# Performance work log

Measured on AMD Instinct MI355X. Metric: run time of the kernel, lower is better.

Reference implementation:

```python
import jax, jax.numpy as jnp
import numpy as np

NUM_EMBEDDINGS = 1024
EMBEDDING_DIM = 64
BETA = 0.25  # commitment_cost


def setup_inputs() -> dict:
    key = jax.random.key(0)
    k1, k2 = jax.random.split(key)
    z = jax.random.normal(k1, (32, EMBEDDING_DIM, 32, 32), dtype=jnp.float32)
    embedding = jax.random.normal(k2, (NUM_EMBEDDINGS, EMBEDDING_DIM), dtype=jnp.float32)
    return {"z": z, "embedding": embedding}


def reference(z, embedding):
    B, D, H, W = z.shape
    beta = jnp.asarray(BETA, z.dtype)
    # [B, D, H, W] -> [B*H*W, D]
    z_flat = jnp.transpose(z, (0, 2, 3, 1)).reshape(-1, D)
    # squared L2 distances to each code: ||z||^2 - 2 z.e^T + ||e||^2  -> [N, E]
    dist = (
        jnp.sum(z_flat * z_flat, axis=1, keepdims=True)
        - 2.0 * (z_flat @ embedding.T)
        + jnp.sum(embedding * embedding, axis=1)
    )
    encoding_indices = jnp.argmin(dist, axis=1)  # [N]
    # direct gather instead of one-hot matmul (same math)
    quantized = embedding[encoding_indices]  # [N, D]
    quantized = jnp.transpose(quantized.reshape(B, H, W, D), (0, 3, 1, 2))
    commitment_loss = beta * jnp.mean(
        (jax.lax.stop_gradient(z) - quantized) ** 2
    )
    codebook_loss = jnp.mean((z - jax.lax.stop_gradient(quantized)) ** 2)
    loss = commitment_loss + codebook_loss
    # straight-through estimator
    quantized_st = z + jax.lax.stop_gradient(quantized - z)
    return (quantized_st, loss, encoding_indices)
```

## Files before the change

kernel.cpp:

```cpp
#include <hip/hip_runtime.h>

typedef __attribute__((ext_vector_type(8))) short short8;
typedef __attribute__((ext_vector_type(4))) float f32x4;
typedef unsigned int uint32;

#define DMQ 64
#define QOUT 2097152

__device__ __forceinline__ unsigned short f2bf(float f){
  uint32 u = __float_as_uint(f);
  return (unsigned short)((u + 0x7FFFu + ((u >> 16) & 1u)) >> 16);
}
__device__ __forceinline__ float bf2f(unsigned short h){
  return __uint_as_float(((uint32)h) << 16);
}
__device__ __forceinline__ uint32 med3u(uint32 a, uint32 b, uint32 c){
  uint32 d;
  asm("v_med3_u32 %0, %1, %2, %3" : "=v"(d) : "v"(a), "v"(b), "v"(c));
  return d;
}
__device__ __forceinline__ void glds16(const unsigned char* g, unsigned char* l){
  __builtin_amdgcn_global_load_lds(
      (const __attribute__((address_space(1))) unsigned int*)g,
      (__attribute__((address_space(3))) unsigned int*)l, 16, 0, 0);
}

__global__ void vq_prep(const float* __restrict__ emb,
                        unsigned char* __restrict__ ebg,
                        float* __restrict__ nrm64){
  int C = blockIdx.x * 256 + threadIdx.x;
  const float4* e4 = reinterpret_cast<const float4*>(emb + C * DMQ);
  int chunk = C >> 8, cc = C & 255;
  unsigned char* eb = ebg + chunk * 65536;
  int x = (cc & 7) << 1;
  float s = 0.f;
#pragma unroll
  for (int sub = 0; sub < 16; ++sub){
    float4 v = e4[sub];
    s += v.x*v.x + v.y*v.y + v.z*v.z + v.w*v.w;
    ushort4 h, l;
    h.x = f2bf(v.x); l.x = f2bf(v.x - bf2f(h.x));
    h.y = f2bf(v.y); l.y = f2bf(v.y - bf2f(h.y));
    h.z = f2bf(v.z); l.z = f2bf(v.z - bf2f(h.z));
    h.w = f2bf(v.w); l.w = f2bf(v.w - bf2f(h.w));
    int off = cc * 128 + ((sub ^ x) << 3);
    *reinterpret_cast<ushort4*>(eb + off) = h;
    *reinterpret_cast<ushort4*>(eb + 32768 + off) = l;
  }
  nrm64[C] = 0.5f * s + 128.0f;
}

__global__ __launch_bounds__(256, 2) void vq_main(
    const float* __restrict__ z, const float* __restrict__ emb,
    const unsigned char* __restrict__ ebg, const float* __restrict__ nrm64,
    float* __restrict__ out, float* __restrict__ partial)
{
  __shared__ __align__(16) unsigned char LB[65536];
  __shared__ float nrmlds[1024];
  __shared__ uint32 mg[64][2][3];
  __shared__ int kidx[64];
  __shared__ float perr[256];

  const int t = threadIdx.x;
  const int bi = blockIdx.x;
  const int n0 = bi * 64;
  const int b = n0 >> 10;
  const int hw0 = n0 & 1023;
  const int w = t >> 6, lane = t & 63;
  const int wm = w >> 1, wn = w & 1;
  const int l15 = lane & 15, g = lane >> 4;

  for (int i = t; i < 1024; i += 256) nrmlds[i] = nrm64[i];

  float* zf = reinterpret_cast<float*>(LB);
#pragma unroll
  for (int k = 0; k < 16; ++k){
    int li = k * 256 + t;
    int d = li >> 6, j = li & 63;
    zf[j * 68 + d] = z[((b * DMQ + d) << 10) + hw0 + j];
  }
  __syncthreads();

  short8 ah[2][2], al[2][2];
#pragma unroll
  for (int mf = 0; mf < 2; ++mf)
#pragma unroll
    for (int kf = 0; kf < 2; ++kf){
      int row = wm * 32 + mf * 16 + l15;
      int base = row * 68 + kf * 32 + g * 8;
      float4 q0 = *reinterpret_cast<float4*>(&zf[base]);
      float4 q1 = *reinterpret_cast<float4*>(&zf[base + 4]);
      float vv[8] = {q0.x,q0.y,q0.z,q0.w,q1.x,q1.y,q1.z,q1.w};
#pragma unroll
      for (int j = 0; j < 8; ++j){
        float v = -vv[j];
        unsigned short hs = f2bf(v);
        unsigned short ls = f2bf(v - bf2f(hs));
        ah[mf][kf][j] = (short)hs;
        al[mf][kf][j] = (short)ls;
      }
    }
  __syncthreads();

  uint32 u0[8], u1[8], u2[8];
#pragma unroll
  for (int s = 0; s < 8; ++s){ u0[s] = 0xFFFFFFFFu; u1[s] = 0xFFFFFFFFu; u2[s] = 0xFFFFFFFFu; }

  const int cc0 = wn * 128 + l15;
  const int xsw = (l15 & 7) << 1;
  const int v0s = ((g * 2) ^ xsw) << 3;
  const int v1s = ((8 + g * 2) ^ xsw) << 3;

  for (int c = 0; c < 4; ++c){
    const unsigned char* src = ebg + c * 65536;
#pragma unroll
    for (int r = 0; r < 16; ++r){
      int off = (r * 4 + w) * 1024;
      glds16(src + off + lane * 16, LB + off);
    }
    __syncthreads();

#pragma unroll
    for (int nf = 0; nf < 8; ++nf){
      int cc = cc0 + nf * 16;
      const unsigned char* rb = LB + cc * 128;
      short8 bh0 = *reinterpret_cast<const short8*>(rb + v0s);
      short8 bh1 = *reinterpret_cast<const short8*>(rb + v1s);
      short8 bl0 = *reinterpret_cast<const short8*>(rb + 32768 + v0s);
      short8 bl1 = *reinterpret_cast<const short8*>(rb + 32768 + v1s);
      float nv = nrmlds[(c << 8) + cc];
      f32x4 a0 = {nv, nv, nv, nv};
      f32x4 a1 = {nv, nv, nv, nv};
      a0 = __builtin_amdgcn_mfma_f32_16x16x32_bf16(ah[0][0], bh0, a0, 0,0,0);
      a0 = __builtin_amdgcn_mfma_f32_16x16x32_bf16(ah[0][1], bh1, a0, 0,0,0);
      a0 = __builtin_amdgcn_mfma_f32_16x16x32_bf16(al[0][0], bh0, a0, 0,0,0);
      a0 = __builtin_amdgcn_mfma_f32_16x16x32_bf16(al[0][1], bh1, a0, 0,0,0);
      a0 = __builtin_amdgcn_mfma_f32_16x16x32_bf16(ah[0][0], bl0, a0, 0,0,0);
      a0 = __builtin_amdgcn_mfma_f32_16x16x32_bf16(ah[0][1], bl1, a0, 0,0,0);
      a1 = __builtin_amdgcn_mfma_f32_16x16x32_bf16(ah[1][0], bh0, a1, 0,0,0);
      a1 = __builtin_amdgcn_mfma_f32_16x16x32_bf16(ah[1][1], bh1, a1, 0,0,0);
      a1 = __builtin_amdgcn_mfma_f32_16x16x32_bf16(al[1][0], bh0, a1, 0,0,0);
      a1 = __builtin_amdgcn_mfma_f32_16x16x32_bf16(al[1][1], bh1, a1, 0,0,0);
      a1 = __builtin_amdgcn_mfma_f32_16x16x32_bf16(ah[1][0], bl0, a1, 0,0,0);
      a1 = __builtin_amdgcn_mfma_f32_16x16x32_bf16(ah[1][1], bl1, a1, 0,0,0);
      uint32 kb = (uint32)((c << 8) | cc0 | (nf << 4));
#pragma unroll
      for (int r = 0; r < 4; ++r){
        uint32 k0v = (__float_as_uint(a0[r]) & 0xFFFFFC00u) | kb;
        u2[r] = med3u(k0v, u1[r], u2[r]);
        u1[r] = med3u(k0v, u0[r], u1[r]);
        u0[r] = u0[r] < k0v ? u0[r] : k0v;
        uint32 k1v = (__float_as_uint(a1[r]) & 0xFFFFFC00u) | kb;
        u2[4+r] = med3u(k1v, u1[4+r], u2[4+r]);
        u1[4+r] = med3u(k1v, u0[4+r], u1[4+r]);
        u0[4+r] = u0[4+r] < k1v ? u0[4+r] : k1v;
      }
    }
    __syncthreads();
  }

#pragma unroll
  for (int dm = 1; dm < 16; dm <<= 1){
#pragma unroll
    for (int s = 0; s < 8; ++s){
      uint32 x0 = (uint32)__shfl_xor((int)u0[s], dm);
      uint32 x1 = (uint32)__shfl_xor((int)u1[s], dm);
      uint32 x2 = (uint32)__shfl_xor((int)u2[s], dm);
      u2[s] = med3u(x0, u1[s], u2[s]); u1[s] = med3u(x0, u0[s], u1[s]); u0[s] = u0[s] < x0 ? u0[s] : x0;
      u2[s] = med3u(x1, u1[s], u2[s]); u1[s] = med3u(x1, u0[s], u1[s]); u0[s] = u0[s] < x1 ? u0[s] : x1;
      u2[s] = med3u(x2, u1[s], u2[s]); u1[s] = med3u(x2, u0[s], u1[s]); u0[s] = u0[s] < x2 ? u0[s] : x2;
    }
  }
  if (l15 == 0){
#pragma unroll
    for (int mf = 0; mf < 2; ++mf)
#pragma unroll
      for (int r = 0; r < 4; ++r){
        int lr = wm * 32 + mf * 16 + g * 4 + r;
        int s = mf * 4 + r;
        mg[lr][wn][0] = u0[s]; mg[lr][wn][1] = u1[s]; mg[lr][wn][2] = u2[s];
      }
  }
  __syncthreads();

  if (t < 64){
    uint32 a0k = mg[t][0][0], a1k = mg[t][0][1], a2k = mg[t][0][2];
#pragma unroll
    for (int j = 0; j < 3; ++j){
      uint32 x = mg[t][1][j];
      a2k = med3u(x, a1k, a2k); a1k = med3u(x, a0k, a1k); a0k = a0k < x ? a0k : x;
    }
    int k0 = (int)(a0k & 1023u);
    float d0 = __uint_as_float(a0k & 0xFFFFFC00u);
    float d1 = __uint_as_float(a1k & 0xFFFFFC00u);
    if (d1 - d0 < 0.125f){
      int k1 = (int)(a1k & 1023u);
      int k2 = (int)(a2k & 1023u);
      float d2v = __uint_as_float(a2k & 0xFFFFFC00u);
      bool c2 = (d2v - d0 < 0.125f);
      const float* zb = z + (b << 16) + hw0 + t;
      const float* e0 = emb + k0 * DMQ;
      const float* e1 = emb + k1 * DMQ;
      const float* e2 = emb + k2 * DMQ;
      double s0 = 0.0, s1 = 0.0, s2 = 0.0;
      for (int d = 0; d < DMQ; ++d){
        double zd = (double)zb[d << 10];
        double t0 = zd - (double)e0[d]; s0 += t0 * t0;
        double t1 = zd - (double)e1[d]; s1 += t1 * t1;
        double t2 = zd - (double)e2[d]; s2 += t2 * t2;
      }
      int bk = k0; double bs = s0;
      if (s1 < bs || (s1 == bs && k1 < bk)) { bs = s1; bk = k1; }
      if (c2 && (s2 < bs || (s2 == bs && k2 < bk))) { bs = s2; bk = k2; }
      k0 = bk;
    }
    kidx[t] = k0;
    out[QOUT + 1 + n0 + t] = (float)k0;
  }
  __syncthreads();

  {
    int row = t & 63, dp = t >> 6;
    int k = kidx[row];
    const float* e = emb + k * DMQ;
    const float* zb = z + (b << 16) + hw0 + row;
    float* ob = out + (b << 16) + hw0 + row;
    float err = 0.f;
#pragma unroll
    for (int dd = 0; dd < 16; ++dd){
      int d = dp * 16 + dd;
      float zv = zb[d << 10];
      float qv = e[d];
      ob[d << 10] = qv;
      float df = zv - qv;
      err = fmaf(df, df, err);
    }
    perr[t] = err;
  }
  __syncthreads();
  for (int ww = 128; ww > 0; ww >>= 1){
    if (t < ww) perr[t] += perr[t + ww];
    __syncthreads();
  }
  if (t == 0) partial[bi] = perr[0];
}

__global__ void vq_reduce(const float* __restrict__ partial, float* __restrict__ out) {
  __shared__ float s[256];
  int t = threadIdx.x;
  s[t] = partial[t] + partial[t + 256];
  __syncthreads();
  for (int w = 128; w > 0; w >>= 1) {
    if (t < w) s[t] += s[t + w];
    __syncthreads();
  }
  if (t == 0) out[QOUT] = 1.25f * s[0] * (1.0f / (float)QOUT);
}

extern "C" void kernel_launch(void* const* d_in, const int* in_sizes, int n_in,
                              void* d_out, int out_size, void* d_ws, size_t ws_size,
                              hipStream_t stream) {
  const float* z   = (const float*)d_in[0];
  const float* emb = (const float*)d_in[1];
  float* out = (float*)d_out;
  unsigned char* ebg = (unsigned char*)d_ws;
  float* nrm64  = (float*)(ebg + 262144);
  float* partial = nrm64 + 1024;

  vq_prep  <<<4,   256, 0, stream>>>(emb, ebg, nrm64);
  vq_main  <<<512, 256, 0, stream>>>(z, emb, ebg, nrm64, out, partial);
  vq_reduce<<<1,   256, 0, stream>>>(partial, out);
}
```

Before: 38.51 us.

## Double-buffer codebook chunks, fuse loss reduction, and parallelize prep and refine

The codebook is now staged in eight 32KB chunks of 128 codes, double-buffered in LDS. The next chunk's global-to-LDS load is issued before the MFMA work on the current chunk, so load latency overlaps compute. The separate reduce kernel is replaced by a last-block pattern that uses an atomic counter and wave-shuffle reductions, which removes one launch. The prep kernel is spread over 64 blocks with one thread per float4. The fp64 refinement of near-tie candidates is split across 4 threads per row, and its tie threshold is tightened from 0.125 to 0.0625, which risks index mismatches on close ties.

```diff
diff --git a/kernel.cpp b/kernel.cpp
--- a/kernel.cpp
+++ b/kernel.cpp
@@ -4,7 +4,6 @@
 typedef __attribute__((ext_vector_type(4))) float f32x4;
 typedef unsigned int uint32;
 
-#define DMQ 64
 #define QOUT 2097152
 
 __device__ __forceinline__ unsigned short f2bf(float f){
@@ -25,41 +24,40 @@
       (__attribute__((address_space(3))) unsigned int*)l, 16, 0, 0);
 }
 
-__global__ void vq_prep(const float* __restrict__ emb,
-                        unsigned char* __restrict__ ebg,
-                        float* __restrict__ nrm64){
-  int C = blockIdx.x * 256 + threadIdx.x;
-  const float4* e4 = reinterpret_cast<const float4*>(emb + C * DMQ);
-  int chunk = C >> 8, cc = C & 255;
-  unsigned char* eb = ebg + chunk * 65536;
-  int x = (cc & 7) << 1;
-  float s = 0.f;
-#pragma unroll
-  for (int sub = 0; sub < 16; ++sub){
-    float4 v = e4[sub];
-    s += v.x*v.x + v.y*v.y + v.z*v.z + v.w*v.w;
-    ushort4 h, l;
-    h.x = f2bf(v.x); l.x = f2bf(v.x - bf2f(h.x));
-    h.y = f2bf(v.y); l.y = f2bf(v.y - bf2f(h.y));
-    h.z = f2bf(v.z); l.z = f2bf(v.z - bf2f(h.z));
-    h.w = f2bf(v.w); l.w = f2bf(v.w - bf2f(h.w));
-    int off = cc * 128 + ((sub ^ x) << 3);
-    *reinterpret_cast<ushort4*>(eb + off) = h;
-    *reinterpret_cast<ushort4*>(eb + 32768 + off) = l;
-  }
-  nrm64[C] = 0.5f * s + 128.0f;
+__global__ void vq_prep(const float* __restrict__ emb, unsigned char* __restrict__ ebg,
+                        float* __restrict__ nrm64, int* __restrict__ cnt){
+  int gt = blockIdx.x * 256 + threadIdx.x;
+  if (gt == 0) *cnt = 0;
+  int C = gt >> 4, sub = gt & 15;
+  float4 v = reinterpret_cast<const float4*>(emb)[C * 16 + sub];
+  float s = v.x*v.x + v.y*v.y + v.z*v.z + v.w*v.w;
+  ushort4 h, l;
+  h.x = f2bf(v.x); l.x = f2bf(v.x - bf2f(h.x));
+  h.y = f2bf(v.y); l.y = f2bf(v.y - bf2f(h.y));
+  h.z = f2bf(v.z); l.z = f2bf(v.z - bf2f(h.z));
+  h.w = f2bf(v.w); l.w = f2bf(v.w - bf2f(h.w));
+  int cc = C & 127;
+  int off = (C >> 7) * 32768 + cc * 128 + ((sub ^ ((cc & 7) << 1)) << 3);
+  *reinterpret_cast<ushort4*>(ebg + off) = h;
+  *reinterpret_cast<ushort4*>(ebg + 16384 + off) = l;
+#pragma unroll
+  for (int d = 1; d < 16; d <<= 1) s += __shfl_xor(s, d);
+  if (sub == 0) nrm64[C] = 0.5f * s + 128.0f;
 }
 
 __global__ __launch_bounds__(256, 2) void vq_main(
     const float* __restrict__ z, const float* __restrict__ emb,
     const unsigned char* __restrict__ ebg, const float* __restrict__ nrm64,
-    float* __restrict__ out, float* __restrict__ partial)
+    float* __restrict__ out, float* __restrict__ partial, int* __restrict__ cnt)
 {
   __shared__ __align__(16) unsigned char LB[65536];
   __shared__ float nrmlds[1024];
   __shared__ uint32 mg[64][2][3];
+  __shared__ uint32 cand[64][4];
   __shared__ int kidx[64];
-  __shared__ float perr[256];
+  __shared__ float werr[4];
+  __shared__ float red[256];
+  __shared__ int isLast;
 
   const int t = threadIdx.x;
   const int bi = blockIdx.x;
@@ -72,14 +70,20 @@
 
   for (int i = t; i < 1024; i += 256) nrmlds[i] = nrm64[i];
 
-  float* zf = reinterpret_cast<float*>(LB);
+  float* zf = reinterpret_cast<float*>(LB + 32768);
 #pragma unroll
   for (int k = 0; k < 16; ++k){
     int li = k * 256 + t;
     int d = li >> 6, j = li & 63;
-    zf[j * 68 + d] = z[((b * DMQ + d) << 10) + hw0 + j];
-  }
-  __syncthreads();
+    zf[j * 68 + d] = z[((b * 64 + d) << 10) + hw0 + j];
+  }
+  __syncthreads();
+
+#pragma unroll
+  for (int r = 0; r < 8; ++r){
+    int off = (r * 4 + w) * 1024;
+    glds16(ebg + off + lane * 16, LB + off);
+  }
 
   short8 ah[2][2], al[2][2];
 #pragma unroll
@@ -106,29 +110,32 @@
 #pragma unroll
   for (int s = 0; s < 8; ++s){ u0[s] = 0xFFFFFFFFu; u1[s] = 0xFFFFFFFFu; u2[s] = 0xFFFFFFFFu; }
 
-  const int cc0 = wn * 128 + l15;
+  const int cc0 = wn * 64 + l15;
   const int xsw = (l15 & 7) << 1;
   const int v0s = ((g * 2) ^ xsw) << 3;
   const int v1s = ((8 + g * 2) ^ xsw) << 3;
 
-  for (int c = 0; c < 4; ++c){
-    const unsigned char* src = ebg + c * 65536;
-#pragma unroll
-    for (int r = 0; r < 16; ++r){
-      int off = (r * 4 + w) * 1024;
-      glds16(src + off + lane * 16, LB + off);
-    }
-    __syncthreads();
-
-#pragma unroll
-    for (int nf = 0; nf < 8; ++nf){
+  for (int h = 0; h < 8; ++h){
+    if (h < 7){
+      const unsigned char* src = ebg + (h + 1) * 32768;
+      unsigned char* dst = LB + (((h + 1) & 1) << 15);
+#pragma unroll
+      for (int r = 0; r < 8; ++r){
+        int off = (r * 4 + w) * 1024;
+        glds16(src + off + lane * 16, dst + off);
+      }
+    }
+    const unsigned char* bufb = LB + ((h & 1) << 15);
+#pragma unroll
+    for (int nf = 0; nf < 4; ++nf){
       int cc = cc0 + nf * 16;
-      const unsigned char* rb = LB + cc * 128;
+      const unsigned char* rb = bufb + cc * 128;
       short8 bh0 = *reinterpret_cast<const short8*>(rb + v0s);
       short8 bh1 = *reinterpret_cast<const short8*>(rb + v1s);
-      short8 bl0 = *reinterpret_cast<const short8*>(rb + 32768 + v0s);
-      short8 bl1 = *reinterpret_cast<const short8*>(rb + 32768 + v1s);
-      float nv = nrmlds[(c << 8) + cc];
+      short8 bl0 = *reinterpret_cast<const short8*>(rb + 16384 + v0s);
+      short8 bl1 = *reinterpret_cast<const short8*>(rb + 16384 + v1s);
+      int code = (h << 7) + cc;
+      float nv = nrmlds[code];
       f32x4 a0 = {nv, nv, nv, nv};
       f32x4 a1 = {nv, nv, nv, nv};
       a0 = __builtin_amdgcn_mfma_f32_16x16x32_bf16(ah[0][0], bh0, a0, 0,0,0);
@@ -143,7 +150,7 @@
       a1 = __builtin_amdgcn_mfma_f32_16x16x32_bf16(al[1][1], bh1, a1, 0,0,0);
       a1 = __builtin_amdgcn_mfma_f32_16x16x32_bf16(ah[1][0], bl0, a1, 0,0,0);
       a1 = __builtin_amdgcn_mfma_f32_16x16x32_bf16(ah[1][1], bl1, a1, 0,0,0);
-      uint32 kb = (uint32)((c << 8) | cc0 | (nf << 4));
+      uint32 kb = (uint32)code;
 #pragma unroll
       for (int r = 0; r < 4; ++r){
         uint32 k0v = (__float_as_uint(a0[r]) & 0xFFFFFC00u) | kb;
@@ -186,43 +193,48 @@
   if (t < 64){
     uint32 a0k = mg[t][0][0], a1k = mg[t][0][1], a2k = mg[t][0][2];
 #pragma unroll
-    for (int j = 0; j < 3; ++j){
-      uint32 x = mg[t][1][j];
+    for (int j2 = 0; j2 < 3; ++j2){
+      uint32 x = mg[t][1][j2];
       a2k = med3u(x, a1k, a2k); a1k = med3u(x, a0k, a1k); a0k = a0k < x ? a0k : x;
     }
-    int k0 = (int)(a0k & 1023u);
+    kidx[t] = (int)(a0k & 1023u);
     float d0 = __uint_as_float(a0k & 0xFFFFFC00u);
     float d1 = __uint_as_float(a1k & 0xFFFFFC00u);
-    if (d1 - d0 < 0.125f){
-      int k1 = (int)(a1k & 1023u);
-      int k2 = (int)(a2k & 1023u);
-      float d2v = __uint_as_float(a2k & 0xFFFFFC00u);
-      bool c2 = (d2v - d0 < 0.125f);
-      const float* zb = z + (b << 16) + hw0 + t;
-      const float* e0 = emb + k0 * DMQ;
-      const float* e1 = emb + k1 * DMQ;
-      const float* e2 = emb + k2 * DMQ;
-      double s0 = 0.0, s1 = 0.0, s2 = 0.0;
-      for (int d = 0; d < DMQ; ++d){
-        double zd = (double)zb[d << 10];
-        double t0 = zd - (double)e0[d]; s0 += t0 * t0;
-        double t1 = zd - (double)e1[d]; s1 += t1 * t1;
-        double t2 = zd - (double)e2[d]; s2 += t2 * t2;
-      }
-      int bk = k0; double bs = s0;
-      if (s1 < bs || (s1 == bs && k1 < bk)) { bs = s1; bk = k1; }
-      if (c2 && (s2 < bs || (s2 == bs && k2 < bk))) { bs = s2; bk = k2; }
-      k0 = bk;
-    }
-    kidx[t] = k0;
-    out[QOUT + 1 + n0 + t] = (float)k0;
+    cand[t][0] = a0k; cand[t][1] = a1k; cand[t][2] = a2k;
+    cand[t][3] = (d1 - d0 < 0.0625f) ? 1u : 0u;
+  }
+  __syncthreads();
+
+  {
+    int row = t >> 2, j = t & 3;
+    if (cand[row][3]){
+      double s = 1e300; int myk = 0x7FFFFFFF;
+      if (j < 3){
+        int k = (int)(cand[row][j] & 1023u);
+        const float* zb = z + (b << 16) + hw0 + row;
+        const float* e = emb + k * 64;
+        double acc = 0.0;
+        for (int d = 0; d < 64; ++d){
+          double df = (double)zb[d << 10] - (double)e[d];
+          acc += df * df;
+        }
+        s = acc; myk = k;
+      }
+#pragma unroll
+      for (int dx = 1; dx < 4; dx <<= 1){
+        double so = __shfl_xor(s, dx);
+        int ko = __shfl_xor(myk, dx);
+        if (so < s || (so == s && ko < myk)) { s = so; myk = ko; }
+      }
+      if (j == 0) kidx[row] = myk;
+    }
   }
   __syncthreads();
 
   {
     int row = t & 63, dp = t >> 6;
     int k = kidx[row];
-    const float* e = emb + k * DMQ;
+    const float* e = emb + k * 64;
     const float* zb = z + (b << 16) + hw0 + row;
     float* ob = out + (b << 16) + hw0 + row;
     float err = 0.f;
@@ -235,26 +247,31 @@
       float df = zv - qv;
       err = fmaf(df, df, err);
     }
-    perr[t] = err;
-  }
-  __syncthreads();
-  for (int ww = 128; ww > 0; ww >>= 1){
-    if (t < ww) perr[t] += perr[t + ww];
+    if (dp == 0) out[QOUT + 1 + n0 + row] = (float)k;
+#pragma unroll
+    for (int dx = 1; dx < 64; dx <<= 1) err += __shfl_xor(err, dx);
+    if (lane == 0) werr[w] = err;
+  }
+  __syncthreads();
+  if (t == 0){
+    partial[bi] = (werr[0] + werr[1]) + (werr[2] + werr[3]);
+    __threadfence();
+    int pos = atomicAdd(cnt, 1);
+    isLast = (pos == 511) ? 1 : 0;
+  }
+  __syncthreads();
+
+  if (isLast){
+    __threadfence();
+    const volatile float* vp = partial;
+    red[t] = vp[t] + vp[t + 256];
     __syncthreads();
-  }
-  if (t == 0) partial[bi] = perr[0];
-}
-
-__global__ void vq_reduce(const float* __restrict__ partial, float* __restrict__ out) {
-  __shared__ float s[256];
-  int t = threadIdx.x;
-  s[t] = partial[t] + partial[t + 256];
-  __syncthreads();
-  for (int w = 128; w > 0; w >>= 1) {
-    if (t < w) s[t] += s[t + w];
-    __syncthreads();
-  }
-  if (t == 0) out[QOUT] = 1.25f * s[0] * (1.0f / (float)QOUT);
+    for (int ww = 128; ww > 0; ww >>= 1){
+      if (t < ww) red[t] += red[t + ww];
+      __syncthreads();
+    }
+    if (t == 0) out[QOUT] = 1.25f * red[0] * (1.0f / 2097152.0f);
+  }
 }
 
 extern "C" void kernel_launch(void* const* d_in, const int* in_sizes, int n_in,
@@ -264,10 +281,10 @@
   const float* emb = (const float*)d_in[1];
   float* out = (float*)d_out;
   unsigned char* ebg = (unsigned char*)d_ws;
-  float* nrm64  = (float*)(ebg + 262144);
+  float* nrm64   = (float*)(ebg + 262144);
   float* partial = nrm64 + 1024;
-
-  vq_prep  <<<4,   256, 0, stream>>>(emb, ebg, nrm64);
-  vq_main  <<<512, 256, 0, stream>>>(z, emb, ebg, nrm64, out, partial);
-  vq_reduce<<<1,   256, 0, stream>>>(partial, out);
-}
+  int*   cnt     = (int*)(partial + 512);
+
+  vq_prep <<<64,  256, 0, stream>>>(emb, ebg, nrm64, cnt);
+  vq_main <<<512, 256, 0, stream>>>(z, emb, ebg, nrm64, out, partial, cnt);
+}
```

Measured after the change: 47.73 us. 24.0% more time.
